# Performance work log

Hardware: AMD Instinct MI355X
Metric: run time of the kernel (lower is better)

Reference implementation:

```python
import jax, jax.numpy as jnp
import numpy as np

D_MODEL = 1024
NUM_HEADS = 16
HEAD_DIM = D_MODEL // NUM_HEADS
SCALE = HEAD_DIM ** -0.5
RMS_EPS = 1e-6


def setup_inputs() -> dict:
    key = jax.random.key(0)
    ks = jax.random.split(key, 6)
    B, T, S = 2, 1024, 2048
    return {
        "query": jax.random.normal(ks[0], (B, T, D_MODEL), dtype=jnp.float32),
        "context": jax.random.normal(ks[1], (B, S, D_MODEL), dtype=jnp.float32),
        "Wq": jax.random.normal(ks[2], (D_MODEL, D_MODEL), dtype=jnp.float32) * (D_MODEL ** -0.5),
        "Wk": jax.random.normal(ks[3], (D_MODEL, D_MODEL), dtype=jnp.float32) * (D_MODEL ** -0.5),
        "Wv": jax.random.normal(ks[4], (D_MODEL, D_MODEL), dtype=jnp.float32) * (D_MODEL ** -0.5),
        "Wo": jax.random.normal(ks[5], (D_MODEL, D_MODEL), dtype=jnp.float32) * (D_MODEL ** -0.5),
        "rms_weight": jnp.ones((D_MODEL,), dtype=jnp.float32),
    }


def _alibi_bias(T, S, num_heads, dtype):
    # slopes = 1 / 2**((h+1)/H) for h in 0..H-1
    base = jnp.arange(1, num_heads + 1, dtype=dtype)
    slopes = 1.0 / jnp.power(jnp.asarray(2.0, dtype), base / num_heads)  # [H]
    rel = jnp.abs(jnp.arange(T, dtype=dtype)[:, None] - jnp.arange(S, dtype=dtype)[None, :])  # [T,S]
    return -slopes[None, :, None, None] * rel[None, None, :, :]  # [1,H,T,S]


def _rmsnorm(x, w, eps=RMS_EPS):
    ms = jnp.mean(jnp.square(x), axis=-1, keepdims=True)
    return x * jax.lax.rsqrt(ms + eps) * w


def reference(query, context, Wq, Wk, Wv, Wo, rms_weight):
    B, T, D = query.shape
    S = context.shape[1]
    H, hd = NUM_HEADS, HEAD_DIM
    # projections (torch Linear: x @ W.T), split into heads: [B,H,L,hd]
    q = (query @ Wq.T).reshape(B, T, H, hd).transpose(0, 2, 1, 3)
    k = (context @ Wk.T).reshape(B, S, H, hd).transpose(0, 2, 1, 3)
    v = (context @ Wv.T).reshape(B, S, H, hd).transpose(0, 2, 1, 3)
    bias = _alibi_bias(T, S, H, query.dtype)
    scores = jnp.einsum("bhtd,bhsd->bhts", q, k) * SCALE + bias
    attn = jax.nn.softmax(scores, axis=-1)
    out = jnp.einsum("bhts,bhsd->bhtd", attn, v)  # [B,H,T,hd]
    out = out.transpose(0, 2, 1, 3).reshape(B, T, D) @ Wo.T
    return _rmsnorm(query + out, rms_weight)
```

## Files before the change

### kernel.cpp

```cpp
#include <hip/hip_runtime.h>
#include <cstdint>
#include <cstddef>

#define D_MODEL 1024
#define NHEADS  16
#define HDIM    64
#define BATCH   2
#define TQ      1024
#define SKL     2048
#define BAND    32
#define BANDW   128
#define SUSED   1152

typedef __bf16 bf16x8 __attribute__((ext_vector_type(8)));
typedef float  f32x4  __attribute__((ext_vector_type(4)));

__device__ __forceinline__ unsigned short f2bf(float f) {
  union { float f; unsigned int u; } v; v.f = f;
  unsigned int r = v.u + 0x7FFFu + ((v.u >> 16) & 1u);
  return (unsigned short)(r >> 16);
}
__device__ __forceinline__ float bf2f(unsigned short x) {
  union { unsigned int u; float f; } v; v.u = (unsigned int)x << 16;
  return v.f;
}

__device__ __forceinline__ void load_lds16(const void* g, void* l) {
  __builtin_amdgcn_global_load_lds(
      (__attribute__((address_space(1))) void*)(uintptr_t)g,
      (__attribute__((address_space(3))) void*)l,
      16, 0, 0);
}

struct CastArgs {
  const float*    src[7];
  unsigned short* dst[7];
  int bstart[7];
};

__global__ __launch_bounds__(256) void cast_kernel(CastArgs a) {
  int bx = blockIdx.x;
  int seg = 0;
#pragma unroll
  for (int i = 1; i < 7; ++i) seg += (bx >= a.bstart[i]) ? 1 : 0;
  size_t idx = (size_t)(bx - a.bstart[seg]) * 1024 + threadIdx.x * 4;
  float4 v = *(const float4*)(a.src[seg] + idx);
  ushort4 o;
  o.x = f2bf(v.x); o.y = f2bf(v.y); o.z = f2bf(v.z); o.w = f2bf(v.w);
  *(ushort4*)(a.dst[seg] + idx) = o;
}

struct ProjArgs {
  const unsigned short* Aq;
  const unsigned short* Wq;
  const unsigned short* Ac;
  const unsigned short* Wk;
  const unsigned short* Wv;
  unsigned short*       Qp;
  unsigned short*       Kp;
  unsigned short*       Vt;
};

__global__ __launch_bounds__(256)
void gemm_proj(ProjArgs pa) {
  __shared__ unsigned short sbuf[2][16384];
  const int tid = threadIdx.x, lane = tid & 63, w = tid >> 6;
  const int quad = lane >> 4, l16 = lane & 15;
  const int wm = (w >> 1) * 64;
  const int lid = blockIdx.x;

  int bm, bn;
  bool isQ;
  if (lid < 128) {
    isQ = true;
    int xcd = lid & 7, idx = lid >> 3;
    bm = (2 * xcd + (idx & 1)) * 128;
    bn = (idx >> 1) * 128;
  } else {
    isQ = false;
    int l2 = lid - 128;
    int xcd = l2 & 7, idx = l2 >> 3;
    int mt, nt;
    if (idx < 32) { mt = 2 * xcd + (idx & 1); nt = idx >> 1; }
    else          { int j = idx - 32; mt = 16 + (j & 1); nt = xcd * 2 + (j >> 1); }
    bm = mt * 128;
    bn = nt * 64;
  }

  int bb = 0, sloc = 0;
  size_t arow0;
  if (isQ) { arow0 = bm; }
  else { bb = bm / SUSED; sloc = bm - bb * SUSED; arow0 = (size_t)bb * SKL + sloc; }

  const unsigned short* gsrc[8];
  int doff[8];
  {
    const unsigned short* Abase = isQ ? pa.Aq : pa.Ac;
#pragma unroll
    for (int l = 0; l < 4; ++l) {
      int f = l * 256 + tid, row = f >> 3, kc = (f & 7) ^ (row & 7);
      gsrc[l] = Abase + (arow0 + row) * 1024 + kc * 8;
      doff[l] = f * 8;
    }
    if (isQ) {
#pragma unroll
      for (int l = 4; l < 8; ++l) {
        int f = (l - 4) * 256 + tid, row = f >> 3, kc = (f & 7) ^ (row & 7);
        gsrc[l] = pa.Wq + (size_t)(bn + row) * 1024 + kc * 8;
        doff[l] = 8192 + f * 8;
      }
    } else {
#pragma unroll
      for (int l = 4; l < 6; ++l) {
        int f = (l - 4) * 256 + tid, row = f >> 3, kc = (f & 7) ^ (row & 7);
        gsrc[l] = pa.Wk + (size_t)(bn + row) * 1024 + kc * 8;
        doff[l] = 8192 + f * 8;
      }
#pragma unroll
      for (int l = 6; l < 8; ++l) {
        int f = (l - 6) * 256 + tid, row = f >> 3, kc = (f & 7) ^ (row & 7);
        gsrc[l] = pa.Wv + (size_t)(bn + row) * 1024 + kc * 8;
        doff[l] = 12288 + f * 8;
      }
    }
  }

  auto stage = [&](int buf, int kk) {
    unsigned short* d = sbuf[buf];
    int ko = kk * 64;
#pragma unroll
    for (int l = 0; l < 8; ++l) load_lds16(gsrc[l] + ko, d + doff[l]);
  };

  const int sw7 = l16 & 7;

  if (isQ) {
    f32x4 acc[4][4];
#pragma unroll
    for (int i = 0; i < 4; ++i)
#pragma unroll
      for (int j = 0; j < 4; ++j) acc[i][j] = (f32x4){0.f, 0.f, 0.f, 0.f};

    stage(0, 0);
    for (int k = 0; k < 16; ++k) {
      if (k) { __asm__ volatile("" ::: "memory"); __builtin_amdgcn_s_barrier(); }
      if (k + 1 < 16) {
        stage((k + 1) & 1, k + 1);
        __asm__ volatile("s_waitcnt vmcnt(8)" ::: "memory");
      } else {
        __asm__ volatile("s_waitcnt vmcnt(0)" ::: "memory");
      }
      __builtin_amdgcn_s_barrier();
      const unsigned short* sb = sbuf[k & 1];
#pragma unroll
      for (int ks = 0; ks < 2; ++ks) {
        int swz = ((ks * 4 + quad) ^ sw7) * 8;
        bf16x8 af[4], bfr[4];
#pragma unroll
        for (int i = 0; i < 4; ++i)
          af[i] = *(const bf16x8*)(sb + (wm + i * 16 + l16) * 64 + swz);
#pragma unroll
        for (int j = 0; j < 4; ++j)
          bfr[j] = *(const bf16x8*)(sb + 8192 + ((w & 1) * 64 + j * 16 + l16) * 64 + swz);
#pragma unroll
        for (int i = 0; i < 4; ++i)
#pragma unroll
          for (int j = 0; j < 4; ++j)
            acc[i][j] = __builtin_amdgcn_mfma_f32_16x16x32_bf16(af[i], bfr[j], acc[i][j], 0, 0, 0);
      }
    }

#pragma unroll
    for (int i = 0; i < 4; ++i)
#pragma unroll
      for (int j = 0; j < 4; ++j)
#pragma unroll
        for (int r = 0; r < 4; ++r)
          pa.Qp[(arow0 + wm + i * 16 + quad * 4 + r) * 1024 +
                bn + (w & 1) * 64 + j * 16 + l16] = f2bf(acc[i][j][r] * 0.125f);
  } else {
    f32x4 acck[4][2], accv[4][2];
#pragma unroll
    for (int i = 0; i < 4; ++i)
#pragma unroll
      for (int j = 0; j < 2; ++j) {
        acck[i][j] = (f32x4){0.f, 0.f, 0.f, 0.f};
        accv[i][j] = (f32x4){0.f, 0.f, 0.f, 0.f};
      }

    stage(0, 0);
    for (int k = 0; k < 16; ++k) {
      if (k) { __asm__ volatile("" ::: "memory"); __builtin_amdgcn_s_barrier(); }
      if (k + 1 < 16) {
        stage((k + 1) & 1, k + 1);
        __asm__ volatile("s_waitcnt vmcnt(8)" ::: "memory");
      } else {
        __asm__ volatile("s_waitcnt vmcnt(0)" ::: "memory");
      }
      __builtin_amdgcn_s_barrier();
      const unsigned short* sb = sbuf[k & 1];
#pragma unroll
      for (int ks = 0; ks < 2; ++ks) {
        int swz = ((ks * 4 + quad) ^ sw7) * 8;
        bf16x8 af[4], bk2[2], bv2[2];
#pragma unroll
        for (int i = 0; i < 4; ++i)
          af[i] = *(const bf16x8*)(sb + (wm + i * 16 + l16) * 64 + swz);
#pragma unroll
        for (int j = 0; j < 2; ++j) {
          int rb = ((w & 1) * 32 + j * 16 + l16) * 64;
          bk2[j] = *(const bf16x8*)(sb + 8192 + rb + swz);
          bv2[j] = *(const bf16x8*)(sb + 12288 + rb + swz);
        }
#pragma unroll
        for (int i = 0; i < 4; ++i)
#pragma unroll
          for (int j = 0; j < 2; ++j) {
            acck[i][j] = __builtin_amdgcn_mfma_f32_16x16x32_bf16(af[i], bk2[j], acck[i][j], 0, 0, 0);
            accv[i][j] = __builtin_amdgcn_mfma_f32_16x16x32_bf16(af[i], bv2[j], accv[i][j], 0, 0, 0);
          }
      }
    }

#pragma unroll
    for (int i = 0; i < 4; ++i) {
#pragma unroll
      for (int j = 0; j < 2; ++j) {
        int col = bn + (w & 1) * 32 + j * 16 + l16;
#pragma unroll
        for (int r = 0; r < 4; ++r)
          pa.Kp[(arow0 + wm + i * 16 + quad * 4 + r) * 1024 + col] = f2bf(acck[i][j][r]);
        int s = sloc + wm + i * 16 + quad * 4;
        ushort4 pk;
        pk.x = f2bf(accv[i][j][0]);
        pk.y = f2bf(accv[i][j][1]);
        pk.z = f2bf(accv[i][j][2]);
        pk.w = f2bf(accv[i][j][3]);
        *(ushort4*)(pa.Vt + ((size_t)bb * 1024 + col) * SKL + s) = pk;
      }
    }
  }
}

__global__ __launch_bounds__(256)
void gemm_out(const unsigned short* __restrict__ A,
              const unsigned short* __restrict__ W,
              unsigned short* __restrict__ Cbase) {
  __shared__ unsigned short sbuf[2][12288];
  const int tid = threadIdx.x, lane = tid & 63, w = tid >> 6;
  const int quad = lane >> 4, l16 = lane & 15;
  const int wm = (w >> 1) * 64, wn = (w & 1) * 32;
  const int xcd = blockIdx.x & 7, idx = blockIdx.x >> 3;
  const size_t bm = (size_t)(2 * xcd + (idx & 1)) * 128;
  const size_t bn = (size_t)((idx >> 1) & 15) * 64;
  const int z = idx >> 5;
  unsigned short* __restrict__ C = Cbase + (size_t)z * TQ * BATCH * 1024;
  const int kbase = z * 512;

  const unsigned short* gsrc[6];
  int doff[6];
#pragma unroll
  for (int l = 0; l < 4; ++l) {
    int f = l * 256 + tid, row = f >> 3, kc = (f & 7) ^ (row & 7);
    gsrc[l] = A + (bm + row) * 1024 + kbase + kc * 8;
    doff[l] = f * 8;
  }
#pragma unroll
  for (int l = 4; l < 6; ++l) {
    int f = (l - 4) * 256 + tid, row = f >> 3, kc = (f & 7) ^ (row & 7);
    gsrc[l] = W + (bn + row) * 1024 + kbase + kc * 8;
    doff[l] = 8192 + f * 8;
  }

  auto stage = [&](int buf, int kk) {
    unsigned short* d = sbuf[buf];
    int ko = kk * 64;
#pragma unroll
    for (int l = 0; l < 6; ++l) load_lds16(gsrc[l] + ko, d + doff[l]);
  };

  const int sw7 = l16 & 7;
  f32x4 acc[4][2];
#pragma unroll
  for (int i = 0; i < 4; ++i)
#pragma unroll
    for (int j = 0; j < 2; ++j) acc[i][j] = (f32x4){0.f, 0.f, 0.f, 0.f};

  stage(0, 0);
  for (int k = 0; k < 8; ++k) {
    if (k) { __asm__ volatile("" ::: "memory"); __builtin_amdgcn_s_barrier(); }
    if (k + 1 < 8) {
      stage((k + 1) & 1, k + 1);
      __asm__ volatile("s_waitcnt vmcnt(6)" ::: "memory");
    } else {
      __asm__ volatile("s_waitcnt vmcnt(0)" ::: "memory");
    }
    __builtin_amdgcn_s_barrier();
    const unsigned short* sb = sbuf[k & 1];
#pragma unroll
    for (int ks = 0; ks < 2; ++ks) {
      int swz = ((ks * 4 + quad) ^ sw7) * 8;
      bf16x8 af[4], bfr[2];
#pragma unroll
      for (int i = 0; i < 4; ++i)
        af[i] = *(const bf16x8*)(sb + (wm + i * 16 + l16) * 64 + swz);
#pragma unroll
      for (int j = 0; j < 2; ++j)
        bfr[j] = *(const bf16x8*)(sb + 8192 + (wn + j * 16 + l16) * 64 + swz);
#pragma unroll
      for (int i = 0; i < 4; ++i)
#pragma unroll
        for (int j = 0; j < 2; ++j)
          acc[i][j] = __builtin_amdgcn_mfma_f32_16x16x32_bf16(af[i], bfr[j], acc[i][j], 0, 0, 0);
    }
  }

#pragma unroll
  for (int i = 0; i < 4; ++i)
#pragma unroll
    for (int j = 0; j < 2; ++j)
#pragma unroll
      for (int r = 0; r < 4; ++r)
        C[(bm + wm + i * 16 + quad * 4 + r) * 1024 + bn + wn + j * 16 + l16] =
            f2bf(acc[i][j][r]);
}

#define PTS 72
#define VCH (BANDW / 8)
__global__ __launch_bounds__(256)
void attn_kernel(const unsigned short* __restrict__ Q,
                 const unsigned short* __restrict__ K,
                 const unsigned short* __restrict__ Vt,
                 unsigned short* __restrict__ O) {
  __shared__ unsigned short sK[BANDW * 64];
  __shared__ unsigned short sV[64 * BANDW];
  __shared__ unsigned short sP[4][16 * PTS];

  const int tid = threadIdx.x, lane = tid & 63, w = tid >> 6;
  const int quad = lane >> 4, l16 = lane & 15;
  const int xcd = blockIdx.x & 7, idx = blockIdx.x >> 3;
  const int g = xcd * 4 + (idx >> 4);
  const int h = idx & 15;
  const int b = g >> 4, bh = b * 16 + h;
  const int q0b = (g & 15) * 64;
  const int q0 = q0b + w * 16;

  const int s_lo = (q0b >= BAND) ? (q0b - BAND) : 0;

  const unsigned short* qrow = Q + (size_t)(b * TQ + q0 + l16) * D_MODEL + h * HDIM;
  bf16x8 qa0 = *(const bf16x8*)(qrow + quad * 8);
  bf16x8 qa1 = *(const bf16x8*)(qrow + 32 + quad * 8);

  const unsigned short* Kbase = K + (size_t)(b * SKL + s_lo) * D_MODEL + h * HDIM;
  const unsigned short* Vbase = Vt + (size_t)bh * HDIM * SKL + s_lo;

#pragma unroll
  for (int it = 0; it < 4; ++it) {
    int flat = it * 256 + tid;
    int row = flat >> 3;
    int kcc = (flat & 7) ^ (row & 7);
    load_lds16(Kbase + (size_t)row * D_MODEL + kcc * 8, sK + flat * 8);
  }
#pragma unroll
  for (int it = 0; it < 4; ++it) {
    int flat = it * 256 + tid;
    int d = flat >> 4;
    int c = flat & 15;
    int cs = c ^ (d & 7);
    load_lds16(Vbase + (size_t)d * SKL + cs * 8, sV + flat * 8);
  }
  __syncthreads();

  float l_lane[4] = {0.f, 0.f, 0.f, 0.f};
  f32x4 o_acc[4];
#pragma unroll
  for (int j = 0; j < 4; ++j) o_acc[j] = (f32x4){0.f, 0.f, 0.f, 0.f};
  const float slope = exp2f(-(float)(h + 1) * (1.0f / NHEADS));
  unsigned short* pw = sP[w];

#pragma unroll
  for (int s0 = 0; s0 < BANDW; s0 += 64) {
    f32x4 sc[4];
#pragma unroll
    for (int n = 0; n < 4; ++n) {
      int srow = s0 + n * 16 + l16;
      int sw = srow & 7;
      bf16x8 kb0 = *(const bf16x8*)(sK + (srow * 8 + (quad ^ sw)) * 8);
      bf16x8 kb1 = *(const bf16x8*)(sK + (srow * 8 + ((4 + quad) ^ sw)) * 8);
      f32x4 zz = (f32x4){0.f, 0.f, 0.f, 0.f};
      zz = __builtin_amdgcn_mfma_f32_16x16x32_bf16(qa0, kb0, zz, 0, 0, 0);
      zz = __builtin_amdgcn_mfma_f32_16x16x32_bf16(qa1, kb1, zz, 0, 0, 0);
      sc[n] = zz;
    }

#pragma unroll
    for (int r = 0; r < 4; ++r) {
      float tpos = (float)(q0 + quad * 4 + r);
#pragma unroll
      for (int n = 0; n < 4; ++n) {
        float spos = (float)(s_lo + s0 + n * 16 + l16);
        float p = __expf(fmaf(-slope, fabsf(tpos - spos), sc[n][r]) - 24.0f);
        sc[n][r] = p;
        l_lane[r] += p;
      }
    }

#pragma unroll
    for (int n = 0; n < 4; ++n)
#pragma unroll
      for (int r = 0; r < 4; ++r)
        pw[(quad * 4 + r) * PTS + n * 16 + l16] = f2bf(sc[n][r]);
    __asm__ volatile("s_waitcnt lgkmcnt(0)" ::: "memory");

    bf16x8 pa0 = *(const bf16x8*)(pw + l16 * PTS + quad * 8);
    bf16x8 pa1 = *(const bf16x8*)(pw + l16 * PTS + 32 + quad * 8);
#pragma unroll
    for (int j = 0; j < 4; ++j) {
      int drow = j * 16 + l16;
      int dw = drow & 7;
      int rb = drow * VCH + (s0 >> 3);
      bf16x8 vb0 = *(const bf16x8*)(sV + (rb + (quad ^ dw)) * 8);
      bf16x8 vb1 = *(const bf16x8*)(sV + (rb + ((4 + quad) ^ dw)) * 8);
      o_acc[j] = __builtin_amdgcn_mfma_f32_16x16x32_bf16(pa0, vb0, o_acc[j], 0, 0, 0);
      o_acc[j] = __builtin_amdgcn_mfma_f32_16x16x32_bf16(pa1, vb1, o_acc[j], 0, 0, 0);
    }
  }

#pragma unroll
  for (int r = 0; r < 4; ++r) {
    float ls = l_lane[r];
    ls += __shfl_xor(ls, 1);
    ls += __shfl_xor(ls, 2);
    ls += __shfl_xor(ls, 4);
    ls += __shfl_xor(ls, 8);
    l_lane[r] = 1.0f / ls;
  }
#pragma unroll
  for (int j = 0; j < 4; ++j)
#pragma unroll
    for (int r = 0; r < 4; ++r)
      O[(size_t)(b * TQ + q0 + quad * 4 + r) * D_MODEL + h * HDIM + j * 16 + l16] =
          f2bf(o_acc[j][r] * l_lane[r]);
}

__global__ __launch_bounds__(256)
void rmsnorm_kernel(const float* __restrict__ q, const unsigned short* __restrict__ p0,
                    const unsigned short* __restrict__ p1, const float* __restrict__ w,
                    float* __restrict__ out) {
  const int row = blockIdx.x, tid = threadIdx.x;
  float4 a = ((const float4*)(q + (size_t)row * 1024))[tid];
  ushort4 u0 = ((const ushort4*)(p0 + (size_t)row * 1024))[tid];
  ushort4 u1 = ((const ushort4*)(p1 + (size_t)row * 1024))[tid];
  float4 y = {a.x + bf2f(u0.x) + bf2f(u1.x), a.y + bf2f(u0.y) + bf2f(u1.y),
              a.z + bf2f(u0.z) + bf2f(u1.z), a.w + bf2f(u0.w) + bf2f(u1.w)};
  float ss = y.x * y.x + y.y * y.y + y.z * y.z + y.w * y.w;
#pragma unroll
  for (int m = 1; m < 64; m <<= 1) ss += __shfl_xor(ss, m);
  __shared__ float sred[4];
  if ((tid & 63) == 0) sred[tid >> 6] = ss;
  __syncthreads();
  float tot = sred[0] + sred[1] + sred[2] + sred[3];
  float rs = rsqrtf(tot * (1.0f / 1024.0f) + 1e-6f);
  float4 wv = ((const float4*)w)[tid];
  float4 o = {y.x * rs * wv.x, y.y * rs * wv.y, y.z * rs * wv.z, y.w * rs * wv.w};
  ((float4*)(out + (size_t)row * 1024))[tid] = o;
}

extern "C" void kernel_launch(void* const* d_in, const int* in_sizes, int n_in,
                              void* d_out, int out_size, void* d_ws, size_t ws_size,
                              hipStream_t stream) {
  (void)in_sizes; (void)n_in; (void)out_size; (void)ws_size;
  const float* query   = (const float*)d_in[0];
  const float* context = (const float*)d_in[1];
  const float* Wq      = (const float*)d_in[2];
  const float* Wk      = (const float*)d_in[3];
  const float* Wv      = (const float*)d_in[4];
  const float* Wo      = (const float*)d_in[5];
  const float* rmsw    = (const float*)d_in[6];

  char* ws = (char*)d_ws;
  unsigned short* qb    = (unsigned short*)(ws + 0);
  unsigned short* cb    = (unsigned short*)(ws + 4194304);
  unsigned short* wqb   = (unsigned short*)(ws + 12582912);
  unsigned short* wkb   = (unsigned short*)(ws + 14680064);
  unsigned short* wvb   = (unsigned short*)(ws + 16777216);
  unsigned short* wob   = (unsigned short*)(ws + 18874368);
  unsigned short* Qp    = (unsigned short*)(ws + 20971520);
  unsigned short* Kp    = (unsigned short*)(ws + 25165824);
  unsigned short* Vt    = (unsigned short*)(ws + 33554432);
  unsigned short* attnb = (unsigned short*)(ws + 41943040);
  unsigned short* proj0 = (unsigned short*)(ws + 46137344);

  CastArgs ca;
  ca.src[0] = query;                   ca.dst[0] = qb;
  ca.src[1] = context;                 ca.dst[1] = cb;
  ca.src[2] = context + 2048 * 1024;   ca.dst[2] = cb + 2048 * 1024;
  ca.src[3] = Wq;                      ca.dst[3] = wqb;
  ca.src[4] = Wk;                      ca.dst[4] = wkb;
  ca.src[5] = Wv;                      ca.dst[5] = wvb;
  ca.src[6] = Wo;                      ca.dst[6] = wob;
  ca.bstart[0] = 0;    ca.bstart[1] = 2048; ca.bstart[2] = 3200;
  ca.bstart[3] = 4352; ca.bstart[4] = 5376; ca.bstart[5] = 6400;
  ca.bstart[6] = 7424;
  cast_kernel<<<8448, 256, 0, stream>>>(ca);

  ProjArgs pa;
  pa.Aq = qb;  pa.Wq = wqb; pa.Qp = Qp;
  pa.Ac = cb;  pa.Wk = wkb; pa.Wv = wvb;
  pa.Kp = Kp;  pa.Vt = Vt;
  gemm_proj<<<416, 256, 0, stream>>>(pa);

  attn_kernel<<<512, 256, 0, stream>>>(Qp, Kp, Vt, attnb);
  gemm_out<<<512, 256, 0, stream>>>(attnb, wob, proj0);
  rmsnorm_kernel<<<2048, 256, 0, stream>>>(query, proj0,
                                           proj0 + (size_t)TQ * BATCH * 1024,
                                           rmsw, (float*)d_out);
}
```

Baseline: 131.2 us.

## Fuse cast, projection, attention, output GEMM and RMSNorm into one persistent kernel

Replaces the five separate launches with one persistent kernel of 512 blocks. The phases (bf16 cast, QKV projection, banded attention, output projection, RMSNorm) are separated by atomic-counter grid barriers, and the barrier counter sits in an unused part of the workspace. The aim is to remove per-launch overhead and the tail gaps between kernels. In exchange it relies on all 512 blocks being resident at once (two blocks per CU), adds spin-wait barrier cost, and forces every phase to share one fixed grid size and LDS allocation.

Result: slower. 297.3 us (+126.6%).

```diff
diff --git a/kernel.cpp b/kernel.cpp
--- a/kernel.cpp
+++ b/kernel.cpp
@@ -11,6 +11,9 @@
 #define BAND    32
 #define BANDW   128
 #define SUSED   1152
+#define PTS     72
+#define VCH     (BANDW / 8)
+#define NB      512
 
 typedef __bf16 bf16x8 __attribute__((ext_vector_type(8)));
 typedef float  f32x4  __attribute__((ext_vector_type(4)));
@@ -32,140 +35,412 @@
       16, 0, 0);
 }
 
-struct CastArgs {
-  const float*    src[7];
-  unsigned short* dst[7];
-  int bstart[7];
+__device__ __forceinline__ void grid_sync(int* bar, int target) {
+  __syncthreads();
+  if (threadIdx.x == 0) {
+    __hip_atomic_fetch_add(bar, 1, __ATOMIC_RELEASE, __HIP_MEMORY_SCOPE_AGENT);
+    while (__hip_atomic_fetch_add(bar, 0, __ATOMIC_RELAXED, __HIP_MEMORY_SCOPE_AGENT) < target)
+      __builtin_amdgcn_s_sleep(8);
+    (void)__hip_atomic_load(bar, __ATOMIC_ACQUIRE, __HIP_MEMORY_SCOPE_AGENT);
+  }
+  __syncthreads();
+}
+
+struct MKArgs {
+  const float* query; const float* context;
+  const float* Wq; const float* Wk; const float* Wv; const float* Wo;
+  const float* rmsw;
+  float* out;
+  unsigned short* qb;  unsigned short* cb;
+  unsigned short* wqb; unsigned short* wkb; unsigned short* wvb; unsigned short* wob;
+  unsigned short* Qp;  unsigned short* Kp;  unsigned short* Vt;
+  unsigned short* attnb; unsigned short* proj0;
+  int* bar;
 };
 
-__global__ __launch_bounds__(256) void cast_kernel(CastArgs a) {
-  int bx = blockIdx.x;
-  int seg = 0;
-#pragma unroll
-  for (int i = 1; i < 7; ++i) seg += (bx >= a.bstart[i]) ? 1 : 0;
-  size_t idx = (size_t)(bx - a.bstart[seg]) * 1024 + threadIdx.x * 4;
-  float4 v = *(const float4*)(a.src[seg] + idx);
-  ushort4 o;
-  o.x = f2bf(v.x); o.y = f2bf(v.y); o.z = f2bf(v.z); o.w = f2bf(v.w);
-  *(ushort4*)(a.dst[seg] + idx) = o;
-}
-
-struct ProjArgs {
-  const unsigned short* Aq;
-  const unsigned short* Wq;
-  const unsigned short* Ac;
-  const unsigned short* Wk;
-  const unsigned short* Wv;
-  unsigned short*       Qp;
-  unsigned short*       Kp;
-  unsigned short*       Vt;
-};
-
-__global__ __launch_bounds__(256)
-void gemm_proj(ProjArgs pa) {
-  __shared__ unsigned short sbuf[2][16384];
-  const int tid = threadIdx.x, lane = tid & 63, w = tid >> 6;
-  const int quad = lane >> 4, l16 = lane & 15;
-  const int wm = (w >> 1) * 64;
-  const int lid = blockIdx.x;
-
-  int bm, bn;
-  bool isQ;
-  if (lid < 128) {
-    isQ = true;
-    int xcd = lid & 7, idx = lid >> 3;
-    bm = (2 * xcd + (idx & 1)) * 128;
-    bn = (idx >> 1) * 128;
-  } else {
-    isQ = false;
-    int l2 = lid - 128;
-    int xcd = l2 & 7, idx = l2 >> 3;
-    int mt, nt;
-    if (idx < 32) { mt = 2 * xcd + (idx & 1); nt = idx >> 1; }
-    else          { int j = idx - 32; mt = 16 + (j & 1); nt = xcd * 2 + (j >> 1); }
-    bm = mt * 128;
-    bn = nt * 64;
+__global__ __launch_bounds__(256, 2)
+void mega(MKArgs a) {
+  __shared__ __align__(16) unsigned short smem[32768];
+  const int tid = threadIdx.x;
+  const int bid = blockIdx.x;
+
+  {
+    for (int vb = bid; vb < 8448; vb += NB) {
+      const float* s; unsigned short* d; int base;
+      if      (vb < 2048) { s = a.query;             d = a.qb;            base = 0;    }
+      else if (vb < 3200) { s = a.context;           d = a.cb;            base = 2048; }
+      else if (vb < 4352) { s = a.context + 2097152; d = a.cb + 2097152;  base = 3200; }
+      else if (vb < 5376) { s = a.Wq;                d = a.wqb;           base = 4352; }
+      else if (vb < 6400) { s = a.Wk;                d = a.wkb;           base = 5376; }
+      else if (vb < 7424) { s = a.Wv;                d = a.wvb;           base = 6400; }
+      else                { s = a.Wo;                d = a.wob;           base = 7424; }
+      size_t idx = (size_t)(vb - base) * 1024 + tid * 4;
+      float4 v = *(const float4*)(s + idx);
+      ushort4 o;
+      o.x = f2bf(v.x); o.y = f2bf(v.y); o.z = f2bf(v.z); o.w = f2bf(v.w);
+      *(ushort4*)(d + idx) = o;
+    }
   }
-
-  int bb = 0, sloc = 0;
-  size_t arow0;
-  if (isQ) { arow0 = bm; }
-  else { bb = bm / SUSED; sloc = bm - bb * SUSED; arow0 = (size_t)bb * SKL + sloc; }
-
-  const unsigned short* gsrc[8];
-  int doff[8];
+  grid_sync(a.bar, NB);
+
+  if (bid < 416) {
+    const int lane = tid & 63, w = tid >> 6;
+    const int quad = lane >> 4, l16 = lane & 15;
+    const int wm = (w >> 1) * 64;
+    const int lid = bid;
+
+    int bm, bn;
+    bool isQ;
+    if (lid < 128) {
+      isQ = true;
+      int xcd = lid & 7, idx = lid >> 3;
+      bm = (2 * xcd + (idx & 1)) * 128;
+      bn = (idx >> 1) * 128;
+    } else {
+      isQ = false;
+      int l2 = lid - 128;
+      int xcd = l2 & 7, idx = l2 >> 3;
+      int mt, nt;
+      if (idx < 32) { mt = 2 * xcd + (idx & 1); nt = idx >> 1; }
+      else          { int j = idx - 32; mt = 16 + (j & 1); nt = xcd * 2 + (j >> 1); }
+      bm = mt * 128;
+      bn = nt * 64;
+    }
+
+    int bb = 0, sloc = 0;
+    size_t arow0;
+    if (isQ) { arow0 = bm; }
+    else { bb = bm / SUSED; sloc = bm - bb * SUSED; arow0 = (size_t)bb * SKL + sloc; }
+
+    const unsigned short* gsrc[8];
+    int doff[8];
+    {
+      const unsigned short* Abase = isQ ? a.qb : a.cb;
+#pragma unroll
+      for (int l = 0; l < 4; ++l) {
+        int f = l * 256 + tid, row = f >> 3, kc = (f & 7) ^ (row & 7);
+        gsrc[l] = Abase + (arow0 + row) * 1024 + kc * 8;
+        doff[l] = f * 8;
+      }
+      if (isQ) {
+#pragma unroll
+        for (int l = 4; l < 8; ++l) {
+          int f = (l - 4) * 256 + tid, row = f >> 3, kc = (f & 7) ^ (row & 7);
+          gsrc[l] = a.wqb + (size_t)(bn + row) * 1024 + kc * 8;
+          doff[l] = 8192 + f * 8;
+        }
+      } else {
+#pragma unroll
+        for (int l = 4; l < 6; ++l) {
+          int f = (l - 4) * 256 + tid, row = f >> 3, kc = (f & 7) ^ (row & 7);
+          gsrc[l] = a.wkb + (size_t)(bn + row) * 1024 + kc * 8;
+          doff[l] = 8192 + f * 8;
+        }
+#pragma unroll
+        for (int l = 6; l < 8; ++l) {
+          int f = (l - 6) * 256 + tid, row = f >> 3, kc = (f & 7) ^ (row & 7);
+          gsrc[l] = a.wvb + (size_t)(bn + row) * 1024 + kc * 8;
+          doff[l] = 12288 + f * 8;
+        }
+      }
+    }
+
+    auto stage = [&](int buf, int kk) {
+      unsigned short* d = smem + buf * 16384;
+      int ko = kk * 64;
+#pragma unroll
+      for (int l = 0; l < 8; ++l) load_lds16(gsrc[l] + ko, d + doff[l]);
+    };
+
+    const int sw7 = l16 & 7;
+
+    if (isQ) {
+      f32x4 acc[4][4];
+#pragma unroll
+      for (int i = 0; i < 4; ++i)
+#pragma unroll
+        for (int j = 0; j < 4; ++j) acc[i][j] = (f32x4){0.f, 0.f, 0.f, 0.f};
+
+      stage(0, 0);
+      for (int k = 0; k < 16; ++k) {
+        if (k) { __asm__ volatile("" ::: "memory"); __builtin_amdgcn_s_barrier(); }
+        if (k + 1 < 16) {
+          stage((k + 1) & 1, k + 1);
+          __asm__ volatile("s_waitcnt vmcnt(8)" ::: "memory");
+        } else {
+          __asm__ volatile("s_waitcnt vmcnt(0)" ::: "memory");
+        }
+        __builtin_amdgcn_s_barrier();
+        const unsigned short* sb = smem + (k & 1) * 16384;
+#pragma unroll
+        for (int ks = 0; ks < 2; ++ks) {
+          int swz = ((ks * 4 + quad) ^ sw7) * 8;
+          bf16x8 af[4], bfr[4];
+#pragma unroll
+          for (int i = 0; i < 4; ++i)
+            af[i] = *(const bf16x8*)(sb + (wm + i * 16 + l16) * 64 + swz);
+#pragma unroll
+          for (int j = 0; j < 4; ++j)
+            bfr[j] = *(const bf16x8*)(sb + 8192 + ((w & 1) * 64 + j * 16 + l16) * 64 + swz);
+#pragma unroll
+          for (int i = 0; i < 4; ++i)
+#pragma unroll
+            for (int j = 0; j < 4; ++j)
+              acc[i][j] = __builtin_amdgcn_mfma_f32_16x16x32_bf16(af[i], bfr[j], acc[i][j], 0, 0, 0);
+        }
+      }
+
+#pragma unroll
+      for (int i = 0; i < 4; ++i)
+#pragma unroll
+        for (int j = 0; j < 4; ++j)
+#pragma unroll
+          for (int r = 0; r < 4; ++r)
+            a.Qp[(arow0 + wm + i * 16 + quad * 4 + r) * 1024 +
+                 bn + (w & 1) * 64 + j * 16 + l16] = f2bf(acc[i][j][r] * 0.125f);
+    } else {
+      f32x4 acck[4][2], accv[4][2];
+#pragma unroll
+      for (int i = 0; i < 4; ++i)
+#pragma unroll
+        for (int j = 0; j < 2; ++j) {
+          acck[i][j] = (f32x4){0.f, 0.f, 0.f, 0.f};
+          accv[i][j] = (f32x4){0.f, 0.f, 0.f, 0.f};
+        }
+
+      stage(0, 0);
+      for (int k = 0; k < 16; ++k) {
+        if (k) { __asm__ volatile("" ::: "memory"); __builtin_amdgcn_s_barrier(); }
+        if (k + 1 < 16) {
+          stage((k + 1) & 1, k + 1);
+          __asm__ volatile("s_waitcnt vmcnt(8)" ::: "memory");
+        } else {
+          __asm__ volatile("s_waitcnt vmcnt(0)" ::: "memory");
+        }
+        __builtin_amdgcn_s_barrier();
+        const unsigned short* sb = smem + (k & 1) * 16384;
+#pragma unroll
+        for (int ks = 0; ks < 2; ++ks) {
+          int swz = ((ks * 4 + quad) ^ sw7) * 8;
+          bf16x8 af[4], bk2[2], bv2[2];
+#pragma unroll
+          for (int i = 0; i < 4; ++i)
+            af[i] = *(const bf16x8*)(sb + (wm + i * 16 + l16) * 64 + swz);
+#pragma unroll
+          for (int j = 0; j < 2; ++j) {
+            int rb = ((w & 1) * 32 + j * 16 + l16) * 64;
+            bk2[j] = *(const bf16x8*)(sb + 8192 + rb + swz);
+            bv2[j] = *(const bf16x8*)(sb + 12288 + rb + swz);
+          }
+#pragma unroll
+          for (int i = 0; i < 4; ++i)
+#pragma unroll
+            for (int j = 0; j < 2; ++j) {
+              acck[i][j] = __builtin_amdgcn_mfma_f32_16x16x32_bf16(af[i], bk2[j], acck[i][j], 0, 0, 0);
+              accv[i][j] = __builtin_amdgcn_mfma_f32_16x16x32_bf16(af[i], bv2[j], accv[i][j], 0, 0, 0);
+            }
+        }
+      }
+
+#pragma unroll
+      for (int i = 0; i < 4; ++i) {
+#pragma unroll
+        for (int j = 0; j < 2; ++j) {
+          int col = bn + (w & 1) * 32 + j * 16 + l16;
+#pragma unroll
+          for (int r = 0; r < 4; ++r)
+            a.Kp[(arow0 + wm + i * 16 + quad * 4 + r) * 1024 + col] = f2bf(acck[i][j][r]);
+          int s = sloc + wm + i * 16 + quad * 4;
+          ushort4 pk;
+          pk.x = f2bf(accv[i][j][0]);
+          pk.y = f2bf(accv[i][j][1]);
+          pk.z = f2bf(accv[i][j][2]);
+          pk.w = f2bf(accv[i][j][3]);
+          *(ushort4*)(a.Vt + ((size_t)bb * 1024 + col) * SKL + s) = pk;
+        }
+      }
+    }
+  }
+  grid_sync(a.bar, 2 * NB);
+
   {
-    const unsigned short* Abase = isQ ? pa.Aq : pa.Ac;
+    unsigned short* sK = smem;
+    unsigned short* sV = smem + 8192;
+    unsigned short* sPb = smem + 16384;
+
+    const int lane = tid & 63, w = tid >> 6;
+    const int quad = lane >> 4, l16 = lane & 15;
+    const int xcd = bid & 7, idx = bid >> 3;
+    const int g = xcd * 4 + (idx >> 4);
+    const int h = idx & 15;
+    const int b = g >> 4, bh = b * 16 + h;
+    const int q0b = (g & 15) * 64;
+    const int q0 = q0b + w * 16;
+
+    const int s_lo = (q0b >= BAND) ? (q0b - BAND) : 0;
+
+    const unsigned short* qrow = a.Qp + (size_t)(b * TQ + q0 + l16) * D_MODEL + h * HDIM;
+    bf16x8 qa0 = *(const bf16x8*)(qrow + quad * 8);
+    bf16x8 qa1 = *(const bf16x8*)(qrow + 32 + quad * 8);
+
+    const unsigned short* Kbase = a.Kp + (size_t)(b * SKL + s_lo) * D_MODEL + h * HDIM;
+    const unsigned short* Vbase = a.Vt + (size_t)bh * HDIM * SKL + s_lo;
+
+#pragma unroll
+    for (int it = 0; it < 4; ++it) {
+      int flat = it * 256 + tid;
+      int row = flat >> 3;
+      int kcc = (flat & 7) ^ (row & 7);
+      load_lds16(Kbase + (size_t)row * D_MODEL + kcc * 8, sK + flat * 8);
+    }
+#pragma unroll
+    for (int it = 0; it < 4; ++it) {
+      int flat = it * 256 + tid;
+      int d = flat >> 4;
+      int c = flat & 15;
+      int cs = c ^ (d & 7);
+      load_lds16(Vbase + (size_t)d * SKL + cs * 8, sV + flat * 8);
+    }
+    __syncthreads();
+
+    float l_lane[4] = {0.f, 0.f, 0.f, 0.f};
+    f32x4 o_acc[4];
+#pragma unroll
+    for (int j = 0; j < 4; ++j) o_acc[j] = (f32x4){0.f, 0.f, 0.f, 0.f};
+    const float slope = exp2f(-(float)(h + 1) * (1.0f / NHEADS));
+    unsigned short* pw = sPb + w * (16 * PTS);
+
+#pragma unroll
+    for (int s0 = 0; s0 < BANDW; s0 += 64) {
+      f32x4 sc[4];
+#pragma unroll
+      for (int n = 0; n < 4; ++n) {
+        int srow = s0 + n * 16 + l16;
+        int sw = srow & 7;
+        bf16x8 kb0 = *(const bf16x8*)(sK + (srow * 8 + (quad ^ sw)) * 8);
+        bf16x8 kb1 = *(const bf16x8*)(sK + (srow * 8 + ((4 + quad) ^ sw)) * 8);
+        f32x4 zz = (f32x4){0.f, 0.f, 0.f, 0.f};
+        zz = __builtin_amdgcn_mfma_f32_16x16x32_bf16(qa0, kb0, zz, 0, 0, 0);
+        zz = __builtin_amdgcn_mfma_f32_16x16x32_bf16(qa1, kb1, zz, 0, 0, 0);
+        sc[n] = zz;
+      }
+
+#pragma unroll
+      for (int r = 0; r < 4; ++r) {
+        float tpos = (float)(q0 + quad * 4 + r);
+#pragma unroll
+        for (int n = 0; n < 4; ++n) {
+          float spos = (float)(s_lo + s0 + n * 16 + l16);
+          float p = __expf(fmaf(-slope, fabsf(tpos - spos), sc[n][r]) - 24.0f);
+          sc[n][r] = p;
+          l_lane[r] += p;
+        }
+      }
+
+#pragma unroll
+      for (int n = 0; n < 4; ++n)
+#pragma unroll
+        for (int r = 0; r < 4; ++r)
+          pw[(quad * 4 + r) * PTS + n * 16 + l16] = f2bf(sc[n][r]);
+      __asm__ volatile("s_waitcnt lgkmcnt(0)" ::: "memory");
+
+      bf16x8 pa0 = *(const bf16x8*)(pw + l16 * PTS + quad * 8);
+      bf16x8 pa1 = *(const bf16x8*)(pw + l16 * PTS + 32 + quad * 8);
+#pragma unroll
+      for (int j = 0; j < 4; ++j) {
+        int drow = j * 16 + l16;
+        int dw = drow & 7;
+        int rb = drow * VCH + (s0 >> 3);
+        bf16x8 vb0 = *(const bf16x8*)(sV + (rb + (quad ^ dw)) * 8);
+        bf16x8 vb1 = *(const bf16x8*)(sV + (rb + ((4 + quad) ^ dw)) * 8);
+        o_acc[j] = __builtin_amdgcn_mfma_f32_16x16x32_bf16(pa0, vb0, o_acc[j], 0, 0, 0);
+        o_acc[j] = __builtin_amdgcn_mfma_f32_16x16x32_bf16(pa1, vb1, o_acc[j], 0, 0, 0);
+      }
+    }
+
+#pragma unroll
+    for (int r = 0; r < 4; ++r) {
+      float ls = l_lane[r];
+      ls += __shfl_xor(ls, 1);
+      ls += __shfl_xor(ls, 2);
+      ls += __shfl_xor(ls, 4);
+      ls += __shfl_xor(ls, 8);
+      l_lane[r] = 1.0f / ls;
+    }
+#pragma unroll
+    for (int j = 0; j < 4; ++j)
+#pragma unroll
+      for (int r = 0; r < 4; ++r)
+        a.attnb[(size_t)(b * TQ + q0 + quad * 4 + r) * D_MODEL + h * HDIM + j * 16 + l16] =
+            f2bf(o_acc[j][r] * l_lane[r]);
+  }
+  grid_sync(a.bar, 3 * NB);
+
+  {
+    const int lane = tid & 63, w = tid >> 6;
+    const int quad = lane >> 4, l16 = lane & 15;
+    const int wm = (w >> 1) * 64, wn = (w & 1) * 32;
+    const int xcd = bid & 7, idx = bid >> 3;
+    const size_t bm = (size_t)(2 * xcd + (idx & 1)) * 128;
+    const size_t bn = (size_t)((idx >> 1) & 15) * 64;
+    const int z = idx >> 5;
+    unsigned short* __restrict__ C = a.proj0 + (size_t)z * TQ * BATCH * 1024;
+    const int kbase = z * 512;
+
+    const unsigned short* gsrc[6];
+    int doff[6];
 #pragma unroll
     for (int l = 0; l < 4; ++l) {
       int f = l * 256 + tid, row = f >> 3, kc = (f & 7) ^ (row & 7);
-      gsrc[l] = Abase + (arow0 + row) * 1024 + kc * 8;
+      gsrc[l] = a.attnb + (bm + row) * 1024 + kbase + kc * 8;
       doff[l] = f * 8;
     }
-    if (isQ) {
-#pragma unroll
-      for (int l = 4; l < 8; ++l) {
-        int f = (l - 4) * 256 + tid, row = f >> 3, kc = (f & 7) ^ (row & 7);
-        gsrc[l] = pa.Wq + (size_t)(bn + row) * 1024 + kc * 8;
-        doff[l] = 8192 + f * 8;
-      }
-    } else {
-#pragma unroll
-      for (int l = 4; l < 6; ++l) {
-        int f = (l - 4) * 256 + tid, row = f >> 3, kc = (f & 7) ^ (row & 7);
-        gsrc[l] = pa.Wk + (size_t)(bn + row) * 1024 + kc * 8;
-        doff[l] = 8192 + f * 8;
-      }
-#pragma unroll
-      for (int l = 6; l < 8; ++l) {
-        int f = (l - 6) * 256 + tid, row = f >> 3, kc = (f & 7) ^ (row & 7);
-        gsrc[l] = pa.Wv + (size_t)(bn + row) * 1024 + kc * 8;
-        doff[l] = 12288 + f * 8;
-      }
-    }
-  }
-
-  auto stage = [&](int buf, int kk) {
-    unsigned short* d = sbuf[buf];
-    int ko = kk * 64;
-#pragma unroll
-    for (int l = 0; l < 8; ++l) load_lds16(gsrc[l] + ko, d + doff[l]);
-  };
-
-  const int sw7 = l16 & 7;
-
-  if (isQ) {
-    f32x4 acc[4][4];
+#pragma unroll
+    for (int l = 4; l < 6; ++l) {
+      int f = (l - 4) * 256 + tid, row = f >> 3, kc = (f & 7) ^ (row & 7);
+      gsrc[l] = a.wob + (size_t)(bn + row) * 1024 + kbase + kc * 8;
+      doff[l] = 8192 + f * 8;
+    }
+
+    auto stage = [&](int buf, int kk) {
+      unsigned short* d = smem + buf * 12288;
+      int ko = kk * 64;
+#pragma unroll
+      for (int l = 0; l < 6; ++l) load_lds16(gsrc[l] + ko, d + doff[l]);
+    };
+
+    const int sw7 = l16 & 7;
+    f32x4 acc[4][2];
 #pragma unroll
     for (int i = 0; i < 4; ++i)
 #pragma unroll
-      for (int j = 0; j < 4; ++j) acc[i][j] = (f32x4){0.f, 0.f, 0.f, 0.f};
+      for (int j = 0; j < 2; ++j) acc[i][j] = (f32x4){0.f, 0.f, 0.f, 0.f};
 
     stage(0, 0);
-    for (int k = 0; k < 16; ++k) {
+    for (int k = 0; k < 8; ++k) {
       if (k) { __asm__ volatile("" ::: "memory"); __builtin_amdgcn_s_barrier(); }
-      if (k + 1 < 16) {
+      if (k + 1 < 8) {
         stage((k + 1) & 1, k + 1);
-        __asm__ volatile("s_waitcnt vmcnt(8)" ::: "memory");
+        __asm__ volatile("s_waitcnt vmcnt(6)" ::: "memory");
       } else {
         __asm__ volatile("s_waitcnt vmcnt(0)" ::: "memory");
       }
       __builtin_amdgcn_s_barrier();
-      const unsigned short* sb = sbuf[k & 1];
+      const unsigned short* sb = smem + (k & 1) * 12288;
 #pragma unroll
       for (int ks = 0; ks < 2; ++ks) {
         int swz = ((ks * 4 + quad) ^ sw7) * 8;
-        bf16x8 af[4], bfr[4];
+        bf16x8 af[4], bfr[2];
 #pragma unroll
         for (int i = 0; i < 4; ++i)
           af[i] = *(const bf16x8*)(sb + (wm + i * 16 + l16) * 64 + swz);
 #pragma unroll
-        for (int j = 0; j < 4; ++j)
-          bfr[j] = *(const bf16x8*)(sb + 8192 + ((w & 1) * 64 + j * 16 + l16) * 64 + swz);
+        for (int j = 0; j < 2; ++j)
+          bfr[j] = *(const bf16x8*)(sb + 8192 + (wn + j * 16 + l16) * 64 + swz);
 #pragma unroll
         for (int i = 0; i < 4; ++i)
 #pragma unroll
-          for (int j = 0; j < 4; ++j)
+          for (int j = 0; j < 2; ++j)
             acc[i][j] = __builtin_amdgcn_mfma_f32_16x16x32_bf16(af[i], bfr[j], acc[i][j], 0, 0, 0);
       }
     }
@@ -173,346 +448,67 @@
 #pragma unroll
     for (int i = 0; i < 4; ++i)
 #pragma unroll
-      for (int j = 0; j < 4; ++j)
+      for (int j = 0; j < 2; ++j)
 #pragma unroll
         for (int r = 0; r < 4; ++r)
-          pa.Qp[(arow0 + wm + i * 16 + quad * 4 + r) * 1024 +
-                bn + (w & 1) * 64 + j * 16 + l16] = f2bf(acc[i][j][r] * 0.125f);
-  } else {
-    f32x4 acck[4][2], accv[4][2];
-#pragma unroll
-    for (int i = 0; i < 4; ++i)
-#pragma unroll
-      for (int j = 0; j < 2; ++j) {
-        acck[i][j] = (f32x4){0.f, 0.f, 0.f, 0.f};
-        accv[i][j] = (f32x4){0.f, 0.f, 0.f, 0.f};
-      }
-
-    stage(0, 0);
-    for (int k = 0; k < 16; ++k) {
-      if (k) { __asm__ volatile("" ::: "memory"); __builtin_amdgcn_s_barrier(); }
-      if (k + 1 < 16) {
-        stage((k + 1) & 1, k + 1);
-        __asm__ volatile("s_waitcnt vmcnt(8)" ::: "memory");
-      } else {
-        __asm__ volatile("s_waitcnt vmcnt(0)" ::: "memory");
-      }
-      __builtin_amdgcn_s_barrier();
-      const unsigned short* sb = sbuf[k & 1];
-#pragma unroll
-      for (int ks = 0; ks < 2; ++ks) {
-        int swz = ((ks * 4 + quad) ^ sw7) * 8;
-        bf16x8 af[4], bk2[2], bv2[2];
-#pragma unroll
-        for (int i = 0; i < 4; ++i)
-          af[i] = *(const bf16x8*)(sb + (wm + i * 16 + l16) * 64 + swz);
-#pragma unroll
-        for (int j = 0; j < 2; ++j) {
-          int rb = ((w & 1) * 32 + j * 16 + l16) * 64;
-          bk2[j] = *(const bf16x8*)(sb + 8192 + rb + swz);
-          bv2[j] = *(const bf16x8*)(sb + 12288 + rb + swz);
-        }
-#pragma unroll
-        for (int i = 0; i < 4; ++i)
-#pragma unroll
-          for (int j = 0; j < 2; ++j) {
-            acck[i][j] = __builtin_amdgcn_mfma_f32_16x16x32_bf16(af[i], bk2[j], acck[i][j], 0, 0, 0);
-            accv[i][j] = __builtin_amdgcn_mfma_f32_16x16x32_bf16(af[i], bv2[j], accv[i][j], 0, 0, 0);
-          }
-      }
-    }
-
-#pragma unroll
-    for (int i = 0; i < 4; ++i) {
-#pragma unroll
-      for (int j = 0; j < 2; ++j) {
-        int col = bn + (w & 1) * 32 + j * 16 + l16;
-#pragma unroll
-        for (int r = 0; r < 4; ++r)
-          pa.Kp[(arow0 + wm + i * 16 + quad * 4 + r) * 1024 + col] = f2bf(acck[i][j][r]);
-        int s = sloc + wm + i * 16 + quad * 4;
-        ushort4 pk;
-        pk.x = f2bf(accv[i][j][0]);
-        pk.y = f2bf(accv[i][j][1]);
-        pk.z = f2bf(accv[i][j][2]);
-        pk.w = f2bf(accv[i][j][3]);
-        *(ushort4*)(pa.Vt + ((size_t)bb * 1024 + col) * SKL + s) = pk;
-      }
-    }
+          C[(bm + wm + i * 16 + quad * 4 + r) * 1024 + bn + wn + j * 16 + l16] =
+              f2bf(acc[i][j][r]);
   }
-}
-
-__global__ __launch_bounds__(256)
-void gemm_out(const unsigned short* __restrict__ A,
-              const unsigned short* __restrict__ W,
-              unsigned short* __restrict__ Cbase) {
-  __shared__ unsigned short sbuf[2][12288];
-  const int tid = threadIdx.x, lane = tid & 63, w = tid >> 6;
-  const int quad = lane >> 4, l16 = lane & 15;
-  const int wm = (w >> 1) * 64, wn = (w & 1) * 32;
-  const int xcd = blockIdx.x & 7, idx = blockIdx.x >> 3;
-  const size_t bm = (size_t)(2 * xcd + (idx & 1)) * 128;
-  const size_t bn = (size_t)((idx >> 1) & 15) * 64;
-  const int z = idx >> 5;
-  unsigned short* __restrict__ C = Cbase + (size_t)z * TQ * BATCH * 1024;
-  const int kbase = z * 512;
-
-  const unsigned short* gsrc[6];
-  int doff[6];
-#pragma unroll
-  for (int l = 0; l < 4; ++l) {
-    int f = l * 256 + tid, row = f >> 3, kc = (f & 7) ^ (row & 7);
-    gsrc[l] = A + (bm + row) * 1024 + kbase + kc * 8;
-    doff[l] = f * 8;
+  grid_sync(a.bar, 4 * NB);
+
+  {
+    float* sred = (float*)smem;
+    for (int row = bid; row < 2048; row += NB) {
+      __syncthreads();
+      float4 qv = ((const float4*)(a.query + (size_t)row * 1024))[tid];
+      ushort4 u0 = ((const ushort4*)(a.proj0 + (size_t)row * 1024))[tid];
+      ushort4 u1 = ((const ushort4*)(a.proj0 + (size_t)(row + 2048) * 1024))[tid];
+      float4 y = {qv.x + bf2f(u0.x) + bf2f(u1.x), qv.y + bf2f(u0.y) + bf2f(u1.y),
+                  qv.z + bf2f(u0.z) + bf2f(u1.z), qv.w + bf2f(u0.w) + bf2f(u1.w)};
+      float ss = y.x * y.x + y.y * y.y + y.z * y.z + y.w * y.w;
+#pragma unroll
+      for (int m = 1; m < 64; m <<= 1) ss += __shfl_xor(ss, m);
+      if ((tid & 63) == 0) sred[tid >> 6] = ss;
+      __syncthreads();
+      float tot = sred[0] + sred[1] + sred[2] + sred[3];
+      float rs = rsqrtf(tot * (1.0f / 1024.0f) + 1e-6f);
+      float4 wv = ((const float4*)a.rmsw)[tid];
+      float4 o = {y.x * rs * wv.x, y.y * rs * wv.y, y.z * rs * wv.z, y.w * rs * wv.w};
+      ((float4*)(a.out + (size_t)row * 1024))[tid] = o;
+    }
   }
-#pragma unroll
-  for (int l = 4; l < 6; ++l) {
-    int f = (l - 4) * 256 + tid, row = f >> 3, kc = (f & 7) ^ (row & 7);
-    gsrc[l] = W + (bn + row) * 1024 + kbase + kc * 8;
-    doff[l] = 8192 + f * 8;
-  }
-
-  auto stage = [&](int buf, int kk) {
-    unsigned short* d = sbuf[buf];
-    int ko = kk * 64;
-#pragma unroll
-    for (int l = 0; l < 6; ++l) load_lds16(gsrc[l] + ko, d + doff[l]);
-  };
-
-  const int sw7 = l16 & 7;
-  f32x4 acc[4][2];
-#pragma unroll
-  for (int i = 0; i < 4; ++i)
-#pragma unroll
-    for (int j = 0; j < 2; ++j) acc[i][j] = (f32x4){0.f, 0.f, 0.f, 0.f};
-
-  stage(0, 0);
-  for (int k = 0; k < 8; ++k) {
-    if (k) { __asm__ volatile("" ::: "memory"); __builtin_amdgcn_s_barrier(); }
-    if (k + 1 < 8) {
-      stage((k + 1) & 1, k + 1);
-      __asm__ volatile("s_waitcnt vmcnt(6)" ::: "memory");
-    } else {
-      __asm__ volatile("s_waitcnt vmcnt(0)" ::: "memory");
-    }
-    __builtin_amdgcn_s_barrier();
-    const unsigned short* sb = sbuf[k & 1];
-#pragma unroll
-    for (int ks = 0; ks < 2; ++ks) {
-      int swz = ((ks * 4 + quad) ^ sw7) * 8;
-      bf16x8 af[4], bfr[2];
-#pragma unroll
-      for (int i = 0; i < 4; ++i)
-        af[i] = *(const bf16x8*)(sb + (wm + i * 16 + l16) * 64 + swz);
-#pragma unroll
-      for (int j = 0; j < 2; ++j)
-        bfr[j] = *(const bf16x8*)(sb + 8192 + (wn + j * 16 + l16) * 64 + swz);
-#pragma unroll
-      for (int i = 0; i < 4; ++i)
-#pragma unroll
-        for (int j = 0; j < 2; ++j)
-          acc[i][j] = __builtin_amdgcn_mfma_f32_16x16x32_bf16(af[i], bfr[j], acc[i][j], 0, 0, 0);
-    }
-  }
-
-#pragma unroll
-  for (int i = 0; i < 4; ++i)
-#pragma unroll
-    for (int j = 0; j < 2; ++j)
-#pragma unroll
-      for (int r = 0; r < 4; ++r)
-        C[(bm + wm + i * 16 + quad * 4 + r) * 1024 + bn + wn + j * 16 + l16] =
-            f2bf(acc[i][j][r]);
-}
-
-#define PTS 72
-#define VCH (BANDW / 8)
-__global__ __launch_bounds__(256)
-void attn_kernel(const unsigned short* __restrict__ Q,
-                 const unsigned short* __restrict__ K,
-                 const unsigned short* __restrict__ Vt,
-                 unsigned short* __restrict__ O) {
-  __shared__ unsigned short sK[BANDW * 64];
-  __shared__ unsigned short sV[64 * BANDW];
-  __shared__ unsigned short sP[4][16 * PTS];
-
-  const int tid = threadIdx.x, lane = tid & 63, w = tid >> 6;
-  const int quad = lane >> 4, l16 = lane & 15;
-  const int xcd = blockIdx.x & 7, idx = blockIdx.x >> 3;
-  const int g = xcd * 4 + (idx >> 4);
-  const int h = idx & 15;
-  const int b = g >> 4, bh = b * 16 + h;
-  const int q0b = (g & 15) * 64;
-  const int q0 = q0b + w * 16;
-
-  const int s_lo = (q0b >= BAND) ? (q0b - BAND) : 0;
-
-  const unsigned short* qrow = Q + (size_t)(b * TQ + q0 + l16) * D_MODEL + h * HDIM;
-  bf16x8 qa0 = *(const bf16x8*)(qrow + quad * 8);
-  bf16x8 qa1 = *(const bf16x8*)(qrow + 32 + quad * 8);
-
-  const unsigned short* Kbase = K + (size_t)(b * SKL + s_lo) * D_MODEL + h * HDIM;
-  const unsigned short* Vbase = Vt + (size_t)bh * HDIM * SKL + s_lo;
-
-#pragma unroll
-  for (int it = 0; it < 4; ++it) {
-    int flat = it * 256 + tid;
-    int row = flat >> 3;
-    int kcc = (flat & 7) ^ (row & 7);
-    load_lds16(Kbase + (size_t)row * D_MODEL + kcc * 8, sK + flat * 8);
-  }
-#pragma unroll
-  for (int it = 0; it < 4; ++it) {
-    int flat = it * 256 + tid;
-    int d = flat >> 4;
-    int c = flat & 15;
-    int cs = c ^ (d & 7);
-    load_lds16(Vbase + (size_t)d * SKL + cs * 8, sV + flat * 8);
-  }
-  __syncthreads();
-
-  float l_lane[4] = {0.f, 0.f, 0.f, 0.f};
-  f32x4 o_acc[4];
-#pragma unroll
-  for (int j = 0; j < 4; ++j) o_acc[j] = (f32x4){0.f, 0.f, 0.f, 0.f};
-  const float slope = exp2f(-(float)(h + 1) * (1.0f / NHEADS));
-  unsigned short* pw = sP[w];
-
-#pragma unroll
-  for (int s0 = 0; s0 < BANDW; s0 += 64) {
-    f32x4 sc[4];
-#pragma unroll
-    for (int n = 0; n < 4; ++n) {
-      int srow = s0 + n * 16 + l16;
-      int sw = srow & 7;
-      bf16x8 kb0 = *(const bf16x8*)(sK + (srow * 8 + (quad ^ sw)) * 8);
-      bf16x8 kb1 = *(const bf16x8*)(sK + (srow * 8 + ((4 + quad) ^ sw)) * 8);
-      f32x4 zz = (f32x4){0.f, 0.f, 0.f, 0.f};
-      zz = __builtin_amdgcn_mfma_f32_16x16x32_bf16(qa0, kb0, zz, 0, 0, 0);
-      zz = __builtin_amdgcn_mfma_f32_16x16x32_bf16(qa1, kb1, zz, 0, 0, 0);
-      sc[n] = zz;
-    }
-
-#pragma unroll
-    for (int r = 0; r < 4; ++r) {
-      float tpos = (float)(q0 + quad * 4 + r);
-#pragma unroll
-      for (int n = 0; n < 4; ++n) {
-        float spos = (float)(s_lo + s0 + n * 16 + l16);
-        float p = __expf(fmaf(-slope, fabsf(tpos - spos), sc[n][r]) - 24.0f);
-        sc[n][r] = p;
-        l_lane[r] += p;
-      }
-    }
-
-#pragma unroll
-    for (int n = 0; n < 4; ++n)
-#pragma unroll
-      for (int r = 0; r < 4; ++r)
-        pw[(quad * 4 + r) * PTS + n * 16 + l16] = f2bf(sc[n][r]);
-    __asm__ volatile("s_waitcnt lgkmcnt(0)" ::: "memory");
-
-    bf16x8 pa0 = *(const bf16x8*)(pw + l16 * PTS + quad * 8);
-    bf16x8 pa1 = *(const bf16x8*)(pw + l16 * PTS + 32 + quad * 8);
-#pragma unroll
-    for (int j = 0; j < 4; ++j) {
-      int drow = j * 16 + l16;
-      int dw = drow & 7;
-      int rb = drow * VCH + (s0 >> 3);
-      bf16x8 vb0 = *(const bf16x8*)(sV + (rb + (quad ^ dw)) * 8);
-      bf16x8 vb1 = *(const bf16x8*)(sV + (rb + ((4 + quad) ^ dw)) * 8);
-      o_acc[j] = __builtin_amdgcn_mfma_f32_16x16x32_bf16(pa0, vb0, o_acc[j], 0, 0, 0);
-      o_acc[j] = __builtin_amdgcn_mfma_f32_16x16x32_bf16(pa1, vb1, o_acc[j], 0, 0, 0);
-    }
-  }
-
-#pragma unroll
-  for (int r = 0; r < 4; ++r) {
-    float ls = l_lane[r];
-    ls += __shfl_xor(ls, 1);
-    ls += __shfl_xor(ls, 2);
-    ls += __shfl_xor(ls, 4);
-    ls += __shfl_xor(ls, 8);
-    l_lane[r] = 1.0f / ls;
-  }
-#pragma unroll
-  for (int j = 0; j < 4; ++j)
-#pragma unroll
-    for (int r = 0; r < 4; ++r)
-      O[(size_t)(b * TQ + q0 + quad * 4 + r) * D_MODEL + h * HDIM + j * 16 + l16] =
-          f2bf(o_acc[j][r] * l_lane[r]);
-}
-
-__global__ __launch_bounds__(256)
-void rmsnorm_kernel(const float* __restrict__ q, const unsigned short* __restrict__ p0,
-                    const unsigned short* __restrict__ p1, const float* __restrict__ w,
-                    float* __restrict__ out) {
-  const int row = blockIdx.x, tid = threadIdx.x;
-  float4 a = ((const float4*)(q + (size_t)row * 1024))[tid];
-  ushort4 u0 = ((const ushort4*)(p0 + (size_t)row * 1024))[tid];
-  ushort4 u1 = ((const ushort4*)(p1 + (size_t)row * 1024))[tid];
-  float4 y = {a.x + bf2f(u0.x) + bf2f(u1.x), a.y + bf2f(u0.y) + bf2f(u1.y),
-              a.z + bf2f(u0.z) + bf2f(u1.z), a.w + bf2f(u0.w) + bf2f(u1.w)};
-  float ss = y.x * y.x + y.y * y.y + y.z * y.z + y.w * y.w;
-#pragma unroll
-  for (int m = 1; m < 64; m <<= 1) ss += __shfl_xor(ss, m);
-  __shared__ float sred[4];
-  if ((tid & 63) == 0) sred[tid >> 6] = ss;
-  __syncthreads();
-  float tot = sred[0] + sred[1] + sred[2] + sred[3];
-  float rs = rsqrtf(tot * (1.0f / 1024.0f) + 1e-6f);
-  float4 wv = ((const float4*)w)[tid];
-  float4 o = {y.x * rs * wv.x, y.y * rs * wv.y, y.z * rs * wv.z, y.w * rs * wv.w};
-  ((float4*)(out + (size_t)row * 1024))[tid] = o;
 }
 
 extern "C" void kernel_launch(void* const* d_in, const int* in_sizes, int n_in,
                               void* d_out, int out_size, void* d_ws, size_t ws_size,
                               hipStream_t stream) {
   (void)in_sizes; (void)n_in; (void)out_size; (void)ws_size;
-  const float* query   = (const float*)d_in[0];
-  const float* context = (const float*)d_in[1];
-  const float* Wq      = (const float*)d_in[2];
-  const float* Wk      = (const float*)d_in[3];
-  const float* Wv      = (const float*)d_in[4];
-  const float* Wo      = (const float*)d_in[5];
-  const float* rmsw    = (const float*)d_in[6];
-
   char* ws = (char*)d_ws;
-  unsigned short* qb    = (unsigned short*)(ws + 0);
-  unsigned short* cb    = (unsigned short*)(ws + 4194304);
-  unsigned short* wqb   = (unsigned short*)(ws + 12582912);
-  unsigned short* wkb   = (unsigned short*)(ws + 14680064);
-  unsigned short* wvb   = (unsigned short*)(ws + 16777216);
-  unsigned short* wob   = (unsigned short*)(ws + 18874368);
-  unsigned short* Qp    = (unsigned short*)(ws + 20971520);
-  unsigned short* Kp    = (unsigned short*)(ws + 25165824);
-  unsigned short* Vt    = (unsigned short*)(ws + 33554432);
-  unsigned short* attnb = (unsigned short*)(ws + 41943040);
-  unsigned short* proj0 = (unsigned short*)(ws + 46137344);
-
-  CastArgs ca;
-  ca.src[0] = query;                   ca.dst[0] = qb;
-  ca.src[1] = context;                 ca.dst[1] = cb;
-  ca.src[2] = context + 2048 * 1024;   ca.dst[2] = cb + 2048 * 1024;
-  ca.src[3] = Wq;                      ca.dst[3] = wqb;
-  ca.src[4] = Wk;                      ca.dst[4] = wkb;
-  ca.src[5] = Wv;                      ca.dst[5] = wvb;
-  ca.src[6] = Wo;                      ca.dst[6] = wob;
-  ca.bstart[0] = 0;    ca.bstart[1] = 2048; ca.bstart[2] = 3200;
-  ca.bstart[3] = 4352; ca.bstart[4] = 5376; ca.bstart[5] = 6400;
-  ca.bstart[6] = 7424;
-  cast_kernel<<<8448, 256, 0, stream>>>(ca);
-
-  ProjArgs pa;
-  pa.Aq = qb;  pa.Wq = wqb; pa.Qp = Qp;
-  pa.Ac = cb;  pa.Wk = wkb; pa.Wv = wvb;
-  pa.Kp = Kp;  pa.Vt = Vt;
-  gemm_proj<<<416, 256, 0, stream>>>(pa);
-
-  attn_kernel<<<512, 256, 0, stream>>>(Qp, Kp, Vt, attnb);
-  gemm_out<<<512, 256, 0, stream>>>(attnb, wob, proj0);
-  rmsnorm_kernel<<<2048, 256, 0, stream>>>(query, proj0,
-                                           proj0 + (size_t)TQ * BATCH * 1024,
-                                           rmsw, (float*)d_out);
+
+  MKArgs a;
+  a.query   = (const float*)d_in[0];
+  a.context = (const float*)d_in[1];
+  a.Wq      = (const float*)d_in[2];
+  a.Wk      = (const float*)d_in[3];
+  a.Wv      = (const float*)d_in[4];
+  a.Wo      = (const float*)d_in[5];
+  a.rmsw    = (const float*)d_in[6];
+  a.out     = (float*)d_out;
+
+  a.qb    = (unsigned short*)(ws + 0);
+  a.cb    = (unsigned short*)(ws + 4194304);
+  a.wqb   = (unsigned short*)(ws + 12582912);
+  a.wkb   = (unsigned short*)(ws + 14680064);
+  a.wvb   = (unsigned short*)(ws + 16777216);
+  a.wob   = (unsigned short*)(ws + 18874368);
+  a.Qp    = (unsigned short*)(ws + 20971520);
+  a.Kp    = (unsigned short*)(ws + 25165824);
+  a.Vt    = (unsigned short*)(ws + 33554432);
+  a.attnb = (unsigned short*)(ws + 41943040);
+  a.proj0 = (unsigned short*)(ws + 46137344);
+
+  a.bar = (int*)(ws + 6553600);
+  hipMemsetAsync(a.bar, 0, 64, stream);
+
+  mega<<<NB, 256, 0, stream>>>(a);
 }
```
